# Performance work log

Hardware: AMD Instinct MI355X
Metric: run time of the kernel (lower is better)

## Reference

```python
import jax, jax.numpy as jnp
import numpy as np

B, F, H, W = 2, 8, 16, 16
S = F * H * W                 # 2048 tokens
DIM, NH = 2048, 16
HD = DIM // NH                # 128
C = HD // 2                   # 64 complex pairs per head
CT = C - 2 * (C // 3)         # 22 temporal freqs
CH = C // 3                   # 21 height / 21 width freqs
L = 1024                      # freq table length
SHIFT = 4                     # TCROPE_SHIFT
EPS = 1e-6


def setup_inputs():
    key = jax.random.key(0)
    ks = jax.random.split(key, 12)
    lin = lambda k: jax.random.normal(k, (DIM, DIM), jnp.float32) / np.sqrt(DIM)
    x = jax.random.normal(ks[0], (B, S, DIM), jnp.float32)
    q_w, k_w, v_w, o_w = lin(ks[1]), lin(ks[2]), lin(ks[3]), lin(ks[4])
    q_b = jax.random.normal(ks[5], (DIM,), jnp.float32) * 0.02
    k_b = jax.random.normal(ks[6], (DIM,), jnp.float32) * 0.02
    v_b = jax.random.normal(ks[7], (DIM,), jnp.float32) * 0.02
    o_b = jax.random.normal(ks[8], (DIM,), jnp.float32) * 0.02
    norm_q_w = jnp.ones((DIM,), jnp.float32)
    norm_k_w = jnp.ones((DIM,), jnp.float32)
    # unit-magnitude complex rotations stored as (cos, sin): [L, C, 2]
    inv = 1.0 / (10000.0 ** (np.arange(C, dtype=np.float32) / C))
    ang = np.arange(L, dtype=np.float32)[:, None] * inv[None, :]
    freqs = jnp.asarray(np.stack([np.cos(ang), np.sin(ang)], axis=-1))
    seq_lens = jnp.full((B,), S, jnp.int32)
    grid_sizes = jnp.tile(jnp.array([[F, H, W]], jnp.int32), (B, 1))
    inner_t = jnp.array([[4, 4], [3, 5]], jnp.int32)  # per-sample shot lengths, sum == F
    return dict(x=x, q_w=q_w, q_b=q_b, k_w=k_w, k_b=k_b, v_w=v_w, v_b=v_b,
                o_w=o_w, o_b=o_b, norm_q_w=norm_q_w, norm_k_w=norm_k_w,
                freqs=freqs, seq_lens=seq_lens, grid_sizes=grid_sizes, inner_t=inner_t)


def _rmsnorm(x, w):
    return x * jax.lax.rsqrt(jnp.mean(x * x, axis=-1, keepdims=True) + EPS) * w


def _rope(x, freqs, inner_t, seq_lens):
    # x: [B,S,NH,HD]; per-sample 3D RoPE over (f,h,w) with per-shot temporal index shift.
    xr = x.reshape(B, S, NH, C, 2)
    f0, f1, f2 = freqs[:, :CT], freqs[:, CT:CT + CH], freqs[:, CT + CH:]
    t = jnp.arange(F)
    # frame t belongs to shot j  =>  temporal freq index = j*SHIFT + t  (matches freq_select)
    shot = jax.vmap(lambda it: jnp.searchsorted(jnp.cumsum(it), t, side='right'))(inner_t)
    t_idx = shot * SHIFT + t[None, :]                                   # [B,F]
    tf = jnp.broadcast_to(f0[t_idx][:, :, None, None], (B, F, H, W, CT, 2))
    hf = jnp.broadcast_to(f1[:H][None, None, :, None], (B, F, H, W, CH, 2))
    wf = jnp.broadcast_to(f2[:W][None, None, None, :], (B, F, H, W, CH, 2))
    fr = jnp.concatenate([tf, hf, wf], axis=-2).reshape(B, S, 1, C, 2)  # [B,S,1,C,2]
    a, b = xr[..., 0], xr[..., 1]
    cr, ci = fr[..., 0], fr[..., 1]
    rot = jnp.stack([a * cr - b * ci, a * ci + b * cr], axis=-1).reshape(B, S, NH, HD)
    # positions past f*h*w are left un-rotated in the original (tail concat)
    keep = (jnp.arange(S)[None, :] < seq_lens[:, None])[:, :, None, None]
    return jnp.where(keep, rot, x)


def reference(x, q_w, q_b, k_w, k_b, v_w, v_b, o_w, o_b,
              norm_q_w, norm_k_w, freqs, seq_lens, grid_sizes, inner_t):
    # grid_sizes is (F,H,W) for every sample; baked in as static constants above.
    q = _rmsnorm(x @ q_w + q_b, norm_q_w).reshape(B, S, NH, HD)
    k = _rmsnorm(x @ k_w + k_b, norm_k_w).reshape(B, S, NH, HD)
    v = (x @ v_w + v_b).reshape(B, S, NH, HD)
    q = _rope(q, freqs, inner_t, seq_lens)
    k = _rope(k, freqs, inner_t, seq_lens)
    scores = jnp.einsum('bqnd,bknd->bnqk', q, k) * (HD ** -0.5)
    kmask = (jnp.arange(S)[None, :] < seq_lens[:, None])[:, None, None, :]
    scores = jnp.where(kmask, scores, -1e30)
    attn = jax.nn.softmax(scores, axis=-1)
    out = jnp.einsum('bnqk,bknd->bqnd', attn, v).reshape(B, S, DIM)
    return out @ o_w + o_b
```

## Files before the change

### kernel.cpp

```cpp
#include <hip/hip_runtime.h>


typedef __attribute__((ext_vector_type(8))) short bf16x8;
typedef __attribute__((ext_vector_type(4))) float f32x4;

__device__ __forceinline__ unsigned short f2bf(float f) {
  unsigned int u = __builtin_bit_cast(unsigned int, f);
  u = (u + 0x7FFFu + ((u >> 16) & 1u)) >> 16;
  return (unsigned short)u;
}
__device__ __forceinline__ float bf2f(unsigned short h) {
  unsigned int u = ((unsigned int)h) << 16;
  return __builtin_bit_cast(float, u);
}

#define GLOAD16(gp, lp)                                                        \
  __builtin_amdgcn_global_load_lds(                                            \
      (__attribute__((address_space(1))) void*)(gp),                           \
      (__attribute__((address_space(3))) void*)(lp), 16, 0, 0)

__global__ __launch_bounds__(256) void k_convert(const float* __restrict__ in,
                                                 unsigned short* __restrict__ out,
                                                 int n8) {
  int i = blockIdx.x * 256 + threadIdx.x;
  const int stride = gridDim.x * 256;
  for (; i < n8; i += stride) {
    const float4* p = (const float4*)in + (size_t)i * 2;
    float4 a = p[0], b = p[1];
    bf16x8 v;
    v[0] = (short)f2bf(a.x); v[1] = (short)f2bf(a.y);
    v[2] = (short)f2bf(a.z); v[3] = (short)f2bf(a.w);
    v[4] = (short)f2bf(b.x); v[5] = (short)f2bf(b.y);
    v[6] = (short)f2bf(b.z); v[7] = (short)f2bf(b.w);
    *(bf16x8*)(out + (size_t)i * 8) = v;
  }
}

__global__ __launch_bounds__(256) void k_transpose(const float* __restrict__ in,
                                                   unsigned short* __restrict__ out,
                                                   int R, int C) {
  __shared__ float tile[32][33];
  const int c0 = blockIdx.x * 32, r0 = blockIdx.y * 32;
  const int tx = threadIdx.x, ty = threadIdx.y;
#pragma unroll
  for (int i = 0; i < 4; i++)
    tile[ty + i * 8][tx] = in[(size_t)(r0 + ty + i * 8) * C + c0 + tx];
  __syncthreads();
#pragma unroll
  for (int i = 0; i < 4; i++)
    out[(size_t)(c0 + ty + i * 8) * R + r0 + tx] = f2bf(tile[tx][ty + i * 8]);
}

template <int OUTF32, int BIASMODE>
__global__ __launch_bounds__(256) void k_gemm(const unsigned short* __restrict__ A,
                                              const unsigned short* __restrict__ BT,
                                              void* __restrict__ Cout,
                                              const float* __restrict__ bias,
                                              int M, int N, int K) {
  __shared__ unsigned short As[128 * 32];
  __shared__ unsigned short Bs[128 * 32];
  const int tid = threadIdx.x;
  const int lane = tid & 63, w = tid >> 6;
  const int g = lane >> 4, cc = lane & 15;
  const int gx = gridDim.x;
  int id = blockIdx.y * gx + blockIdx.x;
  const int tot = gx * gridDim.y;
  id = (id & 7) * (tot >> 3) + (id >> 3);
  const int n0 = (id % gx) * 128, m0 = (id / gx) * 128;
  const int wm = (w >> 1) * 64, wn = (w & 1) * 64;
  f32x4 acc[4][4] = {};
  const unsigned short* Ab = A + (size_t)m0 * K;
  const unsigned short* Bb = BT + (size_t)n0 * K;
  const int r0 = tid >> 2, c0 = (tid & 3) * 8;
  for (int kt = 0; kt < K; kt += 32) {
    GLOAD16(Ab + (size_t)r0 * K + kt + c0, As + tid * 8);
    GLOAD16(Ab + (size_t)(r0 + 64) * K + kt + c0, As + (tid + 256) * 8);
    GLOAD16(Bb + (size_t)r0 * K + kt + c0, Bs + tid * 8);
    GLOAD16(Bb + (size_t)(r0 + 64) * K + kt + c0, Bs + (tid + 256) * 8);
    __syncthreads();
    bf16x8 af[4], bfr[4];
#pragma unroll
    for (int m4 = 0; m4 < 4; m4++)
      af[m4] = *(const bf16x8*)(As + (wm + m4 * 16 + cc) * 32 + g * 8);
#pragma unroll
    for (int n4 = 0; n4 < 4; n4++)
      bfr[n4] = *(const bf16x8*)(Bs + (wn + n4 * 16 + cc) * 32 + g * 8);
#pragma unroll
    for (int m4 = 0; m4 < 4; m4++)
#pragma unroll
      for (int n4 = 0; n4 < 4; n4++)
        acc[m4][n4] = __builtin_amdgcn_mfma_f32_16x16x32_bf16(af[m4], bfr[n4],
                                                              acc[m4][n4], 0, 0, 0);
    __syncthreads();
  }
#pragma unroll
  for (int m4 = 0; m4 < 4; m4++)
#pragma unroll
    for (int n4 = 0; n4 < 4; n4++) {
      const int col = n0 + wn + n4 * 16 + cc;
#pragma unroll
      for (int r = 0; r < 4; r++) {
        const int row = m0 + wm + m4 * 16 + g * 4 + r;
        float v = acc[m4][n4][r];
        if (BIASMODE == 1) v += bias[row];
        if (BIASMODE == 2) v += bias[col];
        if (OUTF32)
          ((float*)Cout)[(size_t)row * N + col] = v;
        else
          ((unsigned short*)Cout)[(size_t)row * N + col] = f2bf(v);
      }
    }
}

__device__ __forceinline__ void stage_half(const unsigned short* __restrict__ src,
                                           int K, unsigned short* dst, int tid) {
#pragma unroll
  for (int j = 0; j < 2; j++) {
    const int li = tid + j * 512;
    const int r = li >> 3;
    const int c16 = (li & 7) ^ (r & 7);
    GLOAD16(src + (size_t)r * K + c16 * 8, (char*)dst + li * 16);
  }
}

__global__ __launch_bounds__(512, 2) void k_gemm_yqk(const unsigned short* __restrict__ A,
                                                     const unsigned short* __restrict__ BT,
                                                     unsigned short* __restrict__ Cout) {
  __shared__ unsigned short As[2][256 * 64];
  __shared__ unsigned short Bs[2][256 * 64];
  const int tid = threadIdx.x;
  const int lane = tid & 63, w = tid >> 6;
  const int g = lane >> 4, cc = lane & 15;
  const int wm = (w >> 2) * 128, wn = (w & 3) * 64;
  const int swz = (cc & 7) << 4;
  const int N = 4096, K = 2048;
  int id = blockIdx.x;
  id = (id & 7) * 32 + (id >> 3);
  const int m0 = (id >> 4) * 256, n0 = (id & 15) * 256;
  f32x4 acc[8][4] = {};
  const int T = K >> 6;

  stage_half(BT + (size_t)n0 * K, K, Bs[0], tid);
  stage_half(A + (size_t)m0 * K, K, As[0], tid);
  stage_half(BT + (size_t)(n0 + 128) * K, K, Bs[0] + 8192, tid);
  stage_half(A + (size_t)(m0 + 128) * K, K, As[0] + 8192, tid);
  stage_half(BT + (size_t)n0 * K + 64, K, Bs[1], tid);
  stage_half(A + (size_t)m0 * K + 64, K, As[1], tid);
  asm volatile("s_waitcnt vmcnt(4)" ::: "memory");
  __builtin_amdgcn_s_barrier();

  for (int t = 0; t < T; ++t) {
    const int c = t & 1;
    const char* Ac = (const char*)As[c];
    const char* Bc = (const char*)Bs[c];
    bf16x8 ar[4][2], br[4][2];
#pragma unroll
    for (int m = 0; m < 4; m++)
#pragma unroll
      for (int kk = 0; kk < 2; kk++)
        ar[m][kk] = *(const bf16x8*)(Ac + (wm + m * 16 + cc) * 128 +
                                     ((kk * 64 + g * 16) ^ swz));
#pragma unroll
    for (int n = 0; n < 2; n++)
#pragma unroll
      for (int kk = 0; kk < 2; kk++)
        br[n][kk] = *(const bf16x8*)(Bc + (wn + n * 16 + cc) * 128 +
                                     ((kk * 64 + g * 16) ^ swz));
    stage_half(BT + (size_t)(n0 + 128) * K + ((t + 1) & (T - 1)) * 64, K,
               Bs[c ^ 1] + 8192, tid);
    __builtin_amdgcn_s_barrier();
    asm volatile("s_waitcnt lgkmcnt(0)" ::: "memory");
    __builtin_amdgcn_sched_barrier(0);
    __builtin_amdgcn_s_setprio(1);
#pragma unroll
    for (int kk = 0; kk < 2; kk++)
#pragma unroll
      for (int m = 0; m < 4; m++)
#pragma unroll
        for (int n = 0; n < 2; n++)
          acc[m][n] = __builtin_amdgcn_mfma_f32_16x16x32_bf16(ar[m][kk], br[n][kk],
                                                              acc[m][n], 0, 0, 0);
    __builtin_amdgcn_s_setprio(0);
    __builtin_amdgcn_s_barrier();
#pragma unroll
    for (int n = 2; n < 4; n++)
#pragma unroll
      for (int kk = 0; kk < 2; kk++)
        br[n][kk] = *(const bf16x8*)(Bc + (wn + n * 16 + cc) * 128 +
                                     ((kk * 64 + g * 16) ^ swz));
    stage_half(A + (size_t)(m0 + 128) * K + ((t + 1) & (T - 1)) * 64, K,
               As[c ^ 1] + 8192, tid);
    __builtin_amdgcn_s_barrier();
    asm volatile("s_waitcnt lgkmcnt(0)" ::: "memory");
    __builtin_amdgcn_sched_barrier(0);
    __builtin_amdgcn_s_setprio(1);
#pragma unroll
    for (int kk = 0; kk < 2; kk++)
#pragma unroll
      for (int m = 0; m < 4; m++)
#pragma unroll
        for (int n = 2; n < 4; n++)
          acc[m][n] = __builtin_amdgcn_mfma_f32_16x16x32_bf16(ar[m][kk], br[n][kk],
                                                              acc[m][n], 0, 0, 0);
    __builtin_amdgcn_s_setprio(0);
    __builtin_amdgcn_s_barrier();
#pragma unroll
    for (int m = 0; m < 4; m++)
#pragma unroll
      for (int kk = 0; kk < 2; kk++)
        ar[m][kk] = *(const bf16x8*)(Ac + (wm + (m + 4) * 16 + cc) * 128 +
                                     ((kk * 64 + g * 16) ^ swz));
    stage_half(BT + (size_t)n0 * K + ((t + 2) & (T - 1)) * 64, K, Bs[c], tid);
    __builtin_amdgcn_s_barrier();
    asm volatile("s_waitcnt lgkmcnt(0)" ::: "memory");
    __builtin_amdgcn_sched_barrier(0);
    __builtin_amdgcn_s_setprio(1);
#pragma unroll
    for (int kk = 0; kk < 2; kk++)
#pragma unroll
      for (int m = 0; m < 4; m++)
#pragma unroll
        for (int n = 0; n < 2; n++)
          acc[m + 4][n] = __builtin_amdgcn_mfma_f32_16x16x32_bf16(ar[m][kk], br[n][kk],
                                                                  acc[m + 4][n], 0, 0, 0);
    __builtin_amdgcn_s_setprio(0);
    __builtin_amdgcn_s_barrier();
    stage_half(A + (size_t)m0 * K + ((t + 2) & (T - 1)) * 64, K, As[c], tid);
    __builtin_amdgcn_s_setprio(1);
#pragma unroll
    for (int kk = 0; kk < 2; kk++)
#pragma unroll
      for (int m = 0; m < 4; m++)
#pragma unroll
        for (int n = 2; n < 4; n++)
          acc[m + 4][n] = __builtin_amdgcn_mfma_f32_16x16x32_bf16(ar[m][kk], br[n][kk],
                                                                  acc[m + 4][n], 0, 0, 0);
    __builtin_amdgcn_s_setprio(0);
    if (t < T - 2)
      asm volatile("s_waitcnt vmcnt(4)" ::: "memory");
    else
      asm volatile("s_waitcnt vmcnt(0)" ::: "memory");
    __builtin_amdgcn_sched_barrier(0);
    __builtin_amdgcn_s_barrier();
  }

#pragma unroll
  for (int mi = 0; mi < 8; mi++)
#pragma unroll
    for (int n = 0; n < 4; n++) {
      const int col = n0 + wn + n * 16 + cc;
#pragma unroll
      for (int j = 0; j < 4; j++) {
        const int row = m0 + wm + mi * 16 + g * 4 + j;
        Cout[(size_t)row * N + col] = f2bf(acc[mi][n][j]);
      }
    }
}

__global__ __launch_bounds__(256) void k_qk_epi(const unsigned short* __restrict__ Yqk,
                                                const float* __restrict__ q_b,
                                                const float* __restrict__ k_b,
                                                const float* __restrict__ nqw,
                                                const float* __restrict__ nkw,
                                                const float* __restrict__ freqs,
                                                const int* __restrict__ inner_t,
                                                unsigned short* __restrict__ Q,
                                                unsigned short* __restrict__ K) {
  const int row = blockIdx.x;
  const int b = row >> 11, s = row & 2047;
  const int t = threadIdx.x;
  const unsigned short* yr = Yqk + (size_t)row * 4096;
  bf16x8 yq = *(const bf16x8*)(yr + t * 8);
  bf16x8 yk = *(const bf16x8*)(yr + 2048 + t * 8);
  float4 qb0 = *(const float4*)(q_b + t * 8), qb1 = *(const float4*)(q_b + t * 8 + 4);
  float4 kb0 = *(const float4*)(k_b + t * 8), kb1 = *(const float4*)(k_b + t * 8 + 4);
  float q[8], k[8];
  q[0] = bf2f((unsigned short)yq[0]) + qb0.x; q[1] = bf2f((unsigned short)yq[1]) + qb0.y;
  q[2] = bf2f((unsigned short)yq[2]) + qb0.z; q[3] = bf2f((unsigned short)yq[3]) + qb0.w;
  q[4] = bf2f((unsigned short)yq[4]) + qb1.x; q[5] = bf2f((unsigned short)yq[5]) + qb1.y;
  q[6] = bf2f((unsigned short)yq[6]) + qb1.z; q[7] = bf2f((unsigned short)yq[7]) + qb1.w;
  k[0] = bf2f((unsigned short)yk[0]) + kb0.x; k[1] = bf2f((unsigned short)yk[1]) + kb0.y;
  k[2] = bf2f((unsigned short)yk[2]) + kb0.z; k[3] = bf2f((unsigned short)yk[3]) + kb0.w;
  k[4] = bf2f((unsigned short)yk[4]) + kb1.x; k[5] = bf2f((unsigned short)yk[5]) + kb1.y;
  k[6] = bf2f((unsigned short)yk[6]) + kb1.z; k[7] = bf2f((unsigned short)yk[7]) + kb1.w;
  float ssq = 0.f, ssk = 0.f;
#pragma unroll
  for (int j = 0; j < 8; j++) { ssq += q[j] * q[j]; ssk += k[j] * k[j]; }
#pragma unroll
  for (int off = 32; off; off >>= 1) {
    ssq += __shfl_xor(ssq, off);
    ssk += __shfl_xor(ssk, off);
  }
  __shared__ float red[8];
  const int w = t >> 6;
  if ((t & 63) == 0) { red[w] = ssq; red[4 + w] = ssk; }
  __syncthreads();
  const float sq = red[0] + red[1] + red[2] + red[3];
  const float sk = red[4] + red[5] + red[6] + red[7];
  const float rq = __builtin_amdgcn_rsqf(sq * (1.0f / 2048.0f) + 1e-6f);
  const float rk = __builtin_amdgcn_rsqf(sk * (1.0f / 2048.0f) + 1e-6f);
  float4 nq0 = *(const float4*)(nqw + t * 8), nq1 = *(const float4*)(nqw + t * 8 + 4);
  float4 nk0 = *(const float4*)(nkw + t * 8), nk1 = *(const float4*)(nkw + t * 8 + 4);
  q[0] *= rq * nq0.x; q[1] *= rq * nq0.y; q[2] *= rq * nq0.z; q[3] *= rq * nq0.w;
  q[4] *= rq * nq1.x; q[5] *= rq * nq1.y; q[6] *= rq * nq1.z; q[7] *= rq * nq1.w;
  k[0] *= rk * nk0.x; k[1] *= rk * nk0.y; k[2] *= rk * nk0.z; k[3] *= rk * nk0.w;
  k[4] *= rk * nk1.x; k[5] *= rk * nk1.y; k[6] *= rk * nk1.z; k[7] *= rk * nk1.w;
  const int f = s >> 8, hh = (s >> 4) & 15, ww = s & 15;
  const int it0 = inner_t[b * 2], it1 = inner_t[b * 2 + 1];
  const int trow = ((f >= it0) + (f >= it0 + it1)) * 4 + f;
#pragma unroll
  for (int jj = 0; jj < 4; jj++) {
    const int c = (t * 4 + jj) & 63;
    const int fr = (c < 22) ? trow : ((c < 43) ? hh : ww);
    const float cr = freqs[((size_t)fr * 64 + c) * 2];
    const float ci = freqs[((size_t)fr * 64 + c) * 2 + 1];
    float a = q[2 * jj], bb = q[2 * jj + 1];
    q[2 * jj] = a * cr - bb * ci; q[2 * jj + 1] = a * ci + bb * cr;
    a = k[2 * jj]; bb = k[2 * jj + 1];
    k[2 * jj] = a * cr - bb * ci; k[2 * jj + 1] = a * ci + bb * cr;
  }
  const float QSCALE = 0.08838834764831845f * 1.4426950408889634f;
  bf16x8 oq, ok;
#pragma unroll
  for (int j = 0; j < 8; j++) {
    oq[j] = (short)f2bf(q[j] * QSCALE);
    ok[j] = (short)f2bf(k[j]);
  }
  const int head = t >> 4, d0 = (t & 15) * 8;
  const size_t off = ((size_t)(b * 16 + head) * 2048 + s) * 128 + d0;
  *(bf16x8*)(Q + off) = oq;
  *(bf16x8*)(K + off) = ok;
}

__global__ __launch_bounds__(256) void k_attn(const unsigned short* __restrict__ Q,
                                              const unsigned short* __restrict__ K,
                                              const unsigned short* __restrict__ V,
                                              unsigned short* __restrict__ O) {
  __shared__ unsigned short Ks[2][64 * 128];
  __shared__ unsigned short Vs[2][128 * 64];
  __shared__ unsigned short Ps[4 * 16 * 72];
  const int tid = threadIdx.x;
  const int lane = tid & 63, w = tid >> 6;
  const int g = lane >> 4, cc = lane & 15;
  const int bh = blockIdx.x;
  const int q0 = blockIdx.y * 64;
  const int b = bh >> 4, h = bh & 15;

  const unsigned short* Qb = Q + ((size_t)bh * 2048 + q0 + w * 16 + cc) * 128;
  bf16x8 qf[4];
#pragma unroll
  for (int kk = 0; kk < 4; kk++) qf[kk] = *(const bf16x8*)(Qb + kk * 32 + g * 8);

  const char* kbase = (const char*)(K + (size_t)bh * 2048 * 128);
  const char* vbase = (const char*)V + ((size_t)h * 128 * 4096 + (size_t)b * 2048) * 2;

  f32x4 acc[8] = {};
  float mloc = -3.0e38f, lloc = 0.f;
  unsigned short* Pw = Ps + w * (16 * 72);
  const int gbase = (lane & 48) | (((lane >> 4) & 3) << 2);
  const f32x4 vzero = {0.f, 0.f, 0.f, 0.f};

#define ATTN_STAGE(s0, bi)                                                     \
  {                                                                            \
    const char* kt0 = kbase + (size_t)(s0) * 256;                              \
    const char* vt0 = vbase + (size_t)(s0) * 2;                                \
    char* Kd = (char*)(Ks[bi]);                                                \
    char* Vd = (char*)(Vs[bi]);                                                \
    _Pragma("unroll") for (int i = 0; i < 4; i++) {                            \
      const int li = i * 256 + tid;                                            \
      const int kr = li >> 4;                                                  \
      const int kc = ((li & 15) * 16) ^ ((kr & 7) << 4);                       \
      GLOAD16(kt0 + kr * 256 + kc, Kd + li * 16);                              \
      const int vd = li >> 3;                                                  \
      const int vc = ((li & 7) * 16) ^ ((vd & 7) << 4);                        \
      GLOAD16(vt0 + (size_t)vd * 8192 + vc, Vd + li * 16);                     \
    }                                                                          \
  }

  ATTN_STAGE(0, 0);
  for (int t = 0; t < 32; ++t) {
    const int cur = t & 1;
    if (t < 31) {
      ATTN_STAGE((t + 1) * 64, cur ^ 1);
      asm volatile("s_waitcnt vmcnt(8)" ::: "memory");
    } else {
      asm volatile("s_waitcnt vmcnt(0)" ::: "memory");
    }
    __builtin_amdgcn_sched_barrier(0);
    __builtin_amdgcn_s_barrier();

    const char* kcur = (const char*)(Ks[cur]);
    const int sw = (cc & 7) << 4;
    f32x4 sf[4];
    __builtin_amdgcn_s_setprio(1);
#pragma unroll
    for (int n4 = 0; n4 < 4; n4++) {
      sf[n4] = vzero;
      const char* krow = kcur + (n4 * 16 + cc) * 256;
#pragma unroll
      for (int kk = 0; kk < 4; kk++) {
        bf16x8 kf = *(const bf16x8*)(krow + ((kk * 64 + g * 16) ^ sw));
        sf[n4] = __builtin_amdgcn_mfma_f32_16x16x32_bf16(kf, qf[kk], sf[n4], 0, 0, 0);
      }
    }
    __builtin_amdgcn_s_setprio(0);

    float tm = fmaxf(fmaxf(sf[0][0], sf[0][1]), fmaxf(sf[0][2], sf[0][3]));
#pragma unroll
    for (int n4 = 1; n4 < 4; n4++)
      tm = fmaxf(tm, fmaxf(fmaxf(sf[n4][0], sf[n4][1]), fmaxf(sf[n4][2], sf[n4][3])));
    tm = fmaxf(tm, __shfl_xor(tm, 16));
    tm = fmaxf(tm, __shfl_xor(tm, 32));
    if (__any(tm > mloc + 8.0f)) {
      const float mn = fmaxf(mloc, tm);
      const float sc = __builtin_amdgcn_exp2f(mloc - mn);
      mloc = mn;
      lloc *= sc;
      f32x4 scv;
#pragma unroll
      for (int r = 0; r < 4; r++) scv[r] = __shfl(sc, gbase + r);
#pragma unroll
      for (int d4 = 0; d4 < 8; d4++) acc[d4] *= scv;
    }
    float rs = 0.f;
#pragma unroll
    for (int n4 = 0; n4 < 4; n4++)
#pragma unroll
      for (int r = 0; r < 4; r++) {
        const float p = __builtin_amdgcn_exp2f(sf[n4][r] - mloc);
        rs += p;
        Pw[cc * 72 + n4 * 16 + g * 4 + r] = f2bf(p);
      }
    rs += __shfl_xor(rs, 16);
    rs += __shfl_xor(rs, 32);
    lloc += rs;

    asm volatile("s_waitcnt lgkmcnt(0)" ::: "memory");
    __builtin_amdgcn_sched_barrier(0);

    const char* vcur = (const char*)(Vs[cur]);
    __builtin_amdgcn_s_setprio(1);
#pragma unroll
    for (int ks = 0; ks < 2; ks++) {
      bf16x8 pf = *(const bf16x8*)(Pw + cc * 72 + ks * 32 + g * 8);
#pragma unroll
      for (int d4 = 0; d4 < 8; d4++) {
        const int dd = d4 * 16 + cc;
        bf16x8 vf = *(const bf16x8*)(vcur + dd * 128 +
                                     ((ks * 64 + g * 16) ^ ((dd & 7) << 4)));
        acc[d4] = __builtin_amdgcn_mfma_f32_16x16x32_bf16(pf, vf, acc[d4], 0, 0, 0);
      }
    }
    __builtin_amdgcn_s_setprio(0);

    asm volatile("s_waitcnt lgkmcnt(0)" ::: "memory");
    __builtin_amdgcn_sched_barrier(0);
    __builtin_amdgcn_s_barrier();
  }
#undef ATTN_STAGE

  const float invl = __builtin_amdgcn_rcpf(lloc);
  float ir[4];
#pragma unroll
  for (int r = 0; r < 4; r++) ir[r] = __shfl(invl, gbase + r);
  unsigned short* Ob = O + (size_t)(b * 2048 + q0 + w * 16) * 2048 + h * 128;
#pragma unroll
  for (int d4 = 0; d4 < 8; d4++)
#pragma unroll
    for (int r = 0; r < 4; r++)
      Ob[(size_t)(g * 4 + r) * 2048 + d4 * 16 + cc] = f2bf(acc[d4][r] * ir[r]);
}

extern "C" void kernel_launch(void* const* d_in, const int* in_sizes, int n_in,
                              void* d_out, int out_size, void* d_ws, size_t ws_size,
                              hipStream_t stream) {
  const float* x     = (const float*)d_in[0];
  const float* q_w   = (const float*)d_in[1];
  const float* q_b   = (const float*)d_in[2];
  const float* k_w   = (const float*)d_in[3];
  const float* k_b   = (const float*)d_in[4];
  const float* v_w   = (const float*)d_in[5];
  const float* v_b   = (const float*)d_in[6];
  const float* o_w   = (const float*)d_in[7];
  const float* o_b   = (const float*)d_in[8];
  const float* nqw   = (const float*)d_in[9];
  const float* nkw   = (const float*)d_in[10];
  const float* freqs = (const float*)d_in[11];
  const int* inner_t = (const int*)d_in[14];

  const size_t NEED = (size_t)112 << 20;
  if (ws_size < NEED) return;

  char* ws = (char*)d_ws;
  unsigned short* xb   = (unsigned short*)(ws);
  unsigned short* WqkT = (unsigned short*)(ws + ((size_t)16 << 20));
  unsigned short* WvT  = (unsigned short*)(ws + ((size_t)32 << 20));
  unsigned short* WoT  = (unsigned short*)(ws + ((size_t)40 << 20));
  unsigned short* Yqk  = (unsigned short*)(ws + ((size_t)48 << 20));
  unsigned short* Vt   = (unsigned short*)(ws + ((size_t)80 << 20));
  unsigned short* Kr   = (unsigned short*)(ws + ((size_t)96 << 20));
  unsigned short* Qr   = xb;
  unsigned short* Orow = WqkT;

  dim3 tb(32, 8);
  k_convert<<<2048, 256, 0, stream>>>(x, xb, 4096 * 2048 / 8);
  k_transpose<<<dim3(64, 64), tb, 0, stream>>>(q_w, WqkT, 2048, 2048);
  k_transpose<<<dim3(64, 64), tb, 0, stream>>>(k_w, WqkT + (size_t)2048 * 2048, 2048, 2048);
  k_transpose<<<dim3(64, 64), tb, 0, stream>>>(v_w, WvT, 2048, 2048);
  k_transpose<<<dim3(64, 64), tb, 0, stream>>>(o_w, WoT, 2048, 2048);
  k_gemm_yqk<<<256, 512, 0, stream>>>(xb, WqkT, Yqk);
  k_gemm<0, 1><<<dim3(32, 16), 256, 0, stream>>>(WvT, xb, Vt, v_b, 2048, 4096, 2048);
  k_qk_epi<<<4096, 256, 0, stream>>>(Yqk, q_b, k_b, nqw, nkw, freqs, inner_t, Qr, Kr);
  k_attn<<<dim3(32, 32), 256, 0, stream>>>(Qr, Kr, Vt, Orow);
  k_gemm<1, 2><<<dim3(16, 32), 256, 0, stream>>>(Orow, WoT, (float*)d_out, o_b, 4096, 2048, 2048);
}
```

Before: 354.6 us.

## Use 128-query attention blocks with 8 waves sharing K/V tiles

The attention kernel now runs 512 threads per block covering 128 queries, so each K/V tile staged in LDS is reused by twice as many waves and the total K/V traffic is halved. The grid flips to put query tiles on x. The P scratch buffer switches to an XOR-swizzled layout, packed bf16 conversion is done with v_cvt_pk_bf16_f32, and an explicit lgkmcnt wait before the PV matmul is removed. The trade-off is half as many blocks and heavier per-block synchronization, and dropping the wait relies on compiler ordering for the LDS write/read of P within a wave.

New measurement: 320.2 us. 1.11x faster.

```diff
diff --git a/kernel.cpp b/kernel.cpp
--- a/kernel.cpp
+++ b/kernel.cpp
@@ -332,18 +332,18 @@
   *(bf16x8*)(K + off) = ok;
 }
 
-__global__ __launch_bounds__(256) void k_attn(const unsigned short* __restrict__ Q,
-                                              const unsigned short* __restrict__ K,
-                                              const unsigned short* __restrict__ V,
-                                              unsigned short* __restrict__ O) {
+__global__ __launch_bounds__(512, 4) void k_attn(const unsigned short* __restrict__ Q,
+                                                 const unsigned short* __restrict__ K,
+                                                 const unsigned short* __restrict__ V,
+                                                 unsigned short* __restrict__ O) {
   __shared__ unsigned short Ks[2][64 * 128];
   __shared__ unsigned short Vs[2][128 * 64];
-  __shared__ unsigned short Ps[4 * 16 * 72];
+  __shared__ unsigned short Ps[8 * 16 * 64];
   const int tid = threadIdx.x;
   const int lane = tid & 63, w = tid >> 6;
   const int g = lane >> 4, cc = lane & 15;
-  const int bh = blockIdx.x;
-  const int q0 = blockIdx.y * 64;
+  const int q0 = blockIdx.x * 128;
+  const int bh = blockIdx.y;
   const int b = bh >> 4, h = bh & 15;
 
   const unsigned short* Qb = Q + ((size_t)bh * 2048 + q0 + w * 16 + cc) * 128;
@@ -356,7 +356,8 @@
 
   f32x4 acc[8] = {};
   float mloc = -3.0e38f, lloc = 0.f;
-  unsigned short* Pw = Ps + w * (16 * 72);
+  char* Pb = (char*)Ps + w * 2048 + cc * 128;
+  const int psw = (cc & 7) << 4;
   const int gbase = (lane & 48) | (((lane >> 4) & 3) << 2);
   const f32x4 vzero = {0.f, 0.f, 0.f, 0.f};
 
@@ -366,8 +367,8 @@
     const char* vt0 = vbase + (size_t)(s0) * 2;                                \
     char* Kd = (char*)(Ks[bi]);                                                \
     char* Vd = (char*)(Vs[bi]);                                                \
-    _Pragma("unroll") for (int i = 0; i < 4; i++) {                            \
-      const int li = i * 256 + tid;                                            \
+    _Pragma("unroll") for (int i = 0; i < 2; i++) {                            \
+      const int li = i * 512 + tid;                                            \
       const int kr = li >> 4;                                                  \
       const int kc = ((li & 15) * 16) ^ ((kr & 7) << 4);                       \
       GLOAD16(kt0 + kr * 256 + kc, Kd + li * 16);                              \
@@ -382,7 +383,7 @@
     const int cur = t & 1;
     if (t < 31) {
       ATTN_STAGE((t + 1) * 64, cur ^ 1);
-      asm volatile("s_waitcnt vmcnt(8)" ::: "memory");
+      asm volatile("s_waitcnt vmcnt(4)" ::: "memory");
     } else {
       asm volatile("s_waitcnt vmcnt(0)" ::: "memory");
     }
@@ -405,10 +406,10 @@
     }
     __builtin_amdgcn_s_setprio(0);
 
-    float tm = fmaxf(fmaxf(sf[0][0], sf[0][1]), fmaxf(sf[0][2], sf[0][3]));
-#pragma unroll
-    for (int n4 = 1; n4 < 4; n4++)
-      tm = fmaxf(tm, fmaxf(fmaxf(sf[n4][0], sf[n4][1]), fmaxf(sf[n4][2], sf[n4][3])));
+    float tm = fmaxf(fmaxf(fmaxf(sf[0][0], sf[0][1]), fmaxf(sf[0][2], sf[0][3])),
+                     fmaxf(fmaxf(sf[1][0], sf[1][1]), fmaxf(sf[1][2], sf[1][3])));
+    tm = fmaxf(tm, fmaxf(fmaxf(fmaxf(sf[2][0], sf[2][1]), fmaxf(sf[2][2], sf[2][3])),
+                         fmaxf(fmaxf(sf[3][0], sf[3][1]), fmaxf(sf[3][2], sf[3][3]))));
     tm = fmaxf(tm, __shfl_xor(tm, 16));
     tm = fmaxf(tm, __shfl_xor(tm, 32));
     if (__any(tm > mloc + 8.0f)) {
@@ -424,25 +425,27 @@
     }
     float rs = 0.f;
 #pragma unroll
-    for (int n4 = 0; n4 < 4; n4++)
-#pragma unroll
-      for (int r = 0; r < 4; r++) {
-        const float p = __builtin_amdgcn_exp2f(sf[n4][r] - mloc);
-        rs += p;
-        Pw[cc * 72 + n4 * 16 + g * 4 + r] = f2bf(p);
-      }
+    for (int n4 = 0; n4 < 4; n4++) {
+      const float p0 = __builtin_amdgcn_exp2f(sf[n4][0] - mloc);
+      const float p1 = __builtin_amdgcn_exp2f(sf[n4][1] - mloc);
+      const float p2 = __builtin_amdgcn_exp2f(sf[n4][2] - mloc);
+      const float p3 = __builtin_amdgcn_exp2f(sf[n4][3] - mloc);
+      rs += (p0 + p1) + (p2 + p3);
+      unsigned lo, hi;
+      asm("v_cvt_pk_bf16_f32 %0, %1, %2" : "=v"(lo) : "v"(p0), "v"(p1));
+      asm("v_cvt_pk_bf16_f32 %0, %1, %2" : "=v"(hi) : "v"(p2), "v"(p3));
+      uint2 pv_; pv_.x = lo; pv_.y = hi;
+      *(uint2*)(Pb + ((n4 * 32 + g * 8) ^ psw)) = pv_;
+    }
     rs += __shfl_xor(rs, 16);
     rs += __shfl_xor(rs, 32);
     lloc += rs;
 
-    asm volatile("s_waitcnt lgkmcnt(0)" ::: "memory");
-    __builtin_amdgcn_sched_barrier(0);
-
     const char* vcur = (const char*)(Vs[cur]);
     __builtin_amdgcn_s_setprio(1);
 #pragma unroll
     for (int ks = 0; ks < 2; ks++) {
-      bf16x8 pf = *(const bf16x8*)(Pw + cc * 72 + ks * 32 + g * 8);
+      bf16x8 pf = *(const bf16x8*)(Pb + ((ks * 64 + g * 16) ^ psw));
 #pragma unroll
       for (int d4 = 0; d4 < 8; d4++) {
         const int dd = d4 * 16 + cc;
@@ -511,6 +514,6 @@
   k_gemm_yqk<<<256, 512, 0, stream>>>(xb, WqkT, Yqk);
   k_gemm<0, 1><<<dim3(32, 16), 256, 0, stream>>>(WvT, xb, Vt, v_b, 2048, 4096, 2048);
   k_qk_epi<<<4096, 256, 0, stream>>>(Yqk, q_b, k_b, nqw, nkw, freqs, inner_t, Qr, Kr);
-  k_attn<<<dim3(32, 32), 256, 0, stream>>>(Qr, Kr, Vt, Orow);
+  k_attn<<<dim3(16, 32), 512, 0, stream>>>(Qr, Kr, Vt, Orow);
   k_gemm<1, 2><<<dim3(16, 32), 256, 0, stream>>>(Orow, WoT, (float*)d_out, o_b, 4096, 2048, 2048);
 }
```
